# Kernel tuning notes

Measured on AMD Instinct MI355X. Metric: run time of the kernel, lower is better.

Reference implementation:

```python
import jax, jax.numpy as jnp
import numpy as np

FEAT = 32   # feature_dim
OUT = 4     # out_dim
RES = 128   # resolution per dim (D=H=W)
DO, HO, WO = 1, 2048, 1024  # query point layout


def setup_inputs() -> dict:
    key = jax.random.key(0)
    ks = jax.random.split(key, 10)
    grid = jax.random.uniform(ks[0], (1, FEAT, RES, RES, RES), dtype=jnp.float32)
    coordinate = jax.random.uniform(ks[1], (1, DO, HO, WO, 3), dtype=jnp.float32,
                                    minval=-1.0, maxval=1.0)

    def lin_w(k, fan_in, fan_out):
        # init_weights_normal: normal init scaled by 1/sqrt(fan_in)
        return jax.random.normal(k, (fan_out, fan_in), jnp.float32) * (1.0 / np.sqrt(fan_in))

    w1 = lin_w(ks[2], FEAT, FEAT); b1 = jnp.zeros((FEAT,), jnp.float32)
    w2 = lin_w(ks[3], FEAT, FEAT); b2 = jnp.zeros((FEAT,), jnp.float32)
    w3 = lin_w(ks[4], FEAT, FEAT); b3 = jnp.zeros((FEAT,), jnp.float32)
    w4 = lin_w(ks[5], FEAT, OUT);  b4 = jnp.zeros((OUT,), jnp.float32)
    return {"coordinate": coordinate, "grid": grid,
            "w1": w1, "b1": b1, "w2": w2, "b2": b2,
            "w3": w3, "b3": b3, "w4": w4, "b4": b4}


def _grid_sample3d(grid, coord):
    # grid: (1, C, D, H, W); coord: (1, Do, Ho, Wo, 3) xyz in [-1,1]
    # Matches torch F.grid_sample(mode='bilinear', padding_mode='zeros', align_corners=False)
    # Returns channels-last (1, Do, Ho, Wo, C) (== torch output permuted 0,2,3,4,1).
    _, C, D, H, W = grid.shape
    g = jnp.transpose(grid[0], (1, 2, 3, 0))  # (D, H, W, C)
    out_shape = coord.shape[:-1]
    pts = coord.reshape(-1, 3)
    x, y, z = pts[:, 0], pts[:, 1], pts[:, 2]
    # unnormalize, align_corners=False
    fx = ((x + 1.0) * W - 1.0) * 0.5
    fy = ((y + 1.0) * H - 1.0) * 0.5
    fz = ((z + 1.0) * D - 1.0) * 0.5
    x0f = jnp.floor(fx); y0f = jnp.floor(fy); z0f = jnp.floor(fz)
    tx = fx - x0f; ty = fy - y0f; tz = fz - z0f
    x0 = x0f.astype(jnp.int32); x1 = x0 + 1
    y0 = y0f.astype(jnp.int32); y1 = y0 + 1
    z0 = z0f.astype(jnp.int32); z1 = z0 + 1

    def fetch(zi, yi, xi):
        valid = ((xi >= 0) & (xi < W) & (yi >= 0) & (yi < H) & (zi >= 0) & (zi < D))
        v = g[jnp.clip(zi, 0, D - 1), jnp.clip(yi, 0, H - 1), jnp.clip(xi, 0, W - 1)]  # (N, C)
        return v * valid[:, None].astype(v.dtype)

    wx0, wx1 = (1.0 - tx)[:, None], tx[:, None]
    wy0, wy1 = (1.0 - ty)[:, None], ty[:, None]
    wz0, wz1 = (1.0 - tz)[:, None], tz[:, None]
    out = (fetch(z0, y0, x0) * (wz0 * wy0 * wx0) + fetch(z0, y0, x1) * (wz0 * wy0 * wx1)
         + fetch(z0, y1, x0) * (wz0 * wy1 * wx0) + fetch(z0, y1, x1) * (wz0 * wy1 * wx1)
         + fetch(z1, y0, x0) * (wz1 * wy0 * wx0) + fetch(z1, y0, x1) * (wz1 * wy0 * wx1)
         + fetch(z1, y1, x0) * (wz1 * wy1 * wx0) + fetch(z1, y1, x1) * (wz1 * wy1 * wx1))
    return out.reshape(*out_shape, C)


def reference(coordinate, grid, w1, b1, w2, b2, w3, b3, w4, b4):
    v = _grid_sample3d(grid, coordinate)          # (1, Do, Ho, Wo, FEAT)
    v = jax.nn.relu(v @ w1.T + b1)
    v = jax.nn.relu(v @ w2.T + b2)
    v = jax.nn.relu(v @ w3.T + b3)
    v = v @ w4.T + b4                             # (1, Do, Ho, Wo, OUT)
    return v
```

## Files before the change

kernel.cpp:

```cpp
#include <hip/hip_runtime.h>
#include <cstdint>
#include <cstddef>

#define RES   128
#define FEAT  32
#define NPTS  (2048 * 1024)
#define PLANE ((size_t)RES * RES * RES)

static __device__ __forceinline__ unsigned short f32_to_bf16_rn(float f) {
    unsigned int u = __float_as_uint(f);
    u = (u + 0x7fffu + ((u >> 16) & 1u)) >> 16;
    return (unsigned short)u;
}
static __device__ __forceinline__ float bf16_lo(unsigned int u) {
    return __uint_as_float(u << 16);
}
static __device__ __forceinline__ float bf16_hi(unsigned int u) {
    return __uint_as_float(u & 0xffff0000u);
}

__global__ __launch_bounds__(256) void transpose_grid_kernel(
    const float* __restrict__ g, unsigned short* __restrict__ out)
{
    __shared__ unsigned short lds[64][33];
    const int t  = blockIdx.x;
    const int x0 = (t & 1) * 64;
    const int y  = (t >> 1) & (RES - 1);
    const int z  = t >> 8;
    const int lane = threadIdx.x & 63;
    const int cg   = threadIdx.x >> 6;
    const size_t base = ((size_t)z * RES + y) * RES + x0;

#pragma unroll
    for (int k = 0; k < 8; ++k) {
        const int c = k * 4 + cg;
        const float v = g[(size_t)c * PLANE + base + lane];
        lds[lane][c] = f32_to_bf16_rn(v);
    }
    __syncthreads();

    const int x  = threadIdx.x >> 2;
    const int c0 = (threadIdx.x & 3) * 8;
    const unsigned short* s = &lds[x][c0];
    uint4 pk;
    pk.x = (unsigned int)s[0] | ((unsigned int)s[1] << 16);
    pk.y = (unsigned int)s[2] | ((unsigned int)s[3] << 16);
    pk.z = (unsigned int)s[4] | ((unsigned int)s[5] << 16);
    pk.w = (unsigned int)s[6] | ((unsigned int)s[7] << 16);
    uint4* outv = (uint4*)(out + base * FEAT);
    outv[threadIdx.x] = pk;
}

template <int MODE>
__global__ __launch_bounds__(256) void field_kernel(
    const float* __restrict__ coord,
    const float* __restrict__ grid,
    const unsigned short* __restrict__ tg,
    const float* __restrict__ w1, const float* __restrict__ b1,
    const float* __restrict__ w2, const float* __restrict__ b2,
    const float* __restrict__ w3, const float* __restrict__ b3,
    const float* __restrict__ w4, const float* __restrict__ b4,
    float* __restrict__ out)
{
    const int p = blockIdx.x * 256 + threadIdx.x;

    const float cx = coord[3 * p + 0];
    const float cy = coord[3 * p + 1];
    const float cz = coord[3 * p + 2];

    const float fx = ((cx + 1.0f) * (float)RES - 1.0f) * 0.5f;
    const float fy = ((cy + 1.0f) * (float)RES - 1.0f) * 0.5f;
    const float fz = ((cz + 1.0f) * (float)RES - 1.0f) * 0.5f;

    const float x0f = floorf(fx), y0f = floorf(fy), z0f = floorf(fz);
    const float tx = fx - x0f, ty = fy - y0f, tz = fz - z0f;
    const int x0 = (int)x0f, y0 = (int)y0f, z0 = (int)z0f;

    const float wxa[2] = {1.0f - tx, tx};
    const float wya[2] = {1.0f - ty, ty};
    const float wza[2] = {1.0f - tz, tz};
    const int   xia[2] = {x0, x0 + 1};
    const int   yia[2] = {y0, y0 + 1};
    const int   zia[2] = {z0, z0 + 1};

    float v[FEAT];
#pragma unroll
    for (int c = 0; c < FEAT; ++c) v[c] = 0.0f;

#pragma unroll
    for (int corner = 0; corner < 8; ++corner) {
        const int dx = corner & 1, dy = (corner >> 1) & 1, dz = corner >> 2;
        const int xi = xia[dx], yi = yia[dy], zi = zia[dz];
        const bool valid = (xi >= 0) & (xi < RES) & (yi >= 0) & (yi < RES) &
                           (zi >= 0) & (zi < RES);
        float w = wxa[dx] * wya[dy] * wza[dz];
        w = valid ? w : 0.0f;
        const int xc = min(max(xi, 0), RES - 1);
        const int yc = min(max(yi, 0), RES - 1);
        const int zc = min(max(zi, 0), RES - 1);
        const size_t vox = ((size_t)zc * RES + yc) * RES + xc;

        if (MODE == 1) {
            const uint4* cp = (const uint4*)(tg + vox * FEAT);
#pragma unroll
            for (int q = 0; q < 4; ++q) {
                const uint4 u = cp[q];
                v[q * 8 + 0] = fmaf(w, bf16_lo(u.x), v[q * 8 + 0]);
                v[q * 8 + 1] = fmaf(w, bf16_hi(u.x), v[q * 8 + 1]);
                v[q * 8 + 2] = fmaf(w, bf16_lo(u.y), v[q * 8 + 2]);
                v[q * 8 + 3] = fmaf(w, bf16_hi(u.y), v[q * 8 + 3]);
                v[q * 8 + 4] = fmaf(w, bf16_lo(u.z), v[q * 8 + 4]);
                v[q * 8 + 5] = fmaf(w, bf16_hi(u.z), v[q * 8 + 5]);
                v[q * 8 + 6] = fmaf(w, bf16_lo(u.w), v[q * 8 + 6]);
                v[q * 8 + 7] = fmaf(w, bf16_hi(u.w), v[q * 8 + 7]);
            }
        } else {
#pragma unroll
            for (int c = 0; c < FEAT; ++c)
                v[c] = fmaf(w, grid[(size_t)c * PLANE + vox], v[c]);
        }
    }

    float h[FEAT];
#pragma unroll
    for (int j = 0; j < FEAT; ++j) {
        float a = b1[j];
#pragma unroll
        for (int i = 0; i < FEAT; ++i) a = fmaf(v[i], w1[j * FEAT + i], a);
        h[j] = fmaxf(a, 0.0f);
    }
#pragma unroll
    for (int j = 0; j < FEAT; ++j) {
        float a = b2[j];
#pragma unroll
        for (int i = 0; i < FEAT; ++i) a = fmaf(h[i], w2[j * FEAT + i], a);
        v[j] = fmaxf(a, 0.0f);
    }
#pragma unroll
    for (int j = 0; j < FEAT; ++j) {
        float a = b3[j];
#pragma unroll
        for (int i = 0; i < FEAT; ++i) a = fmaf(v[i], w3[j * FEAT + i], a);
        h[j] = fmaxf(a, 0.0f);
    }
    float r[4];
#pragma unroll
    for (int o = 0; o < 4; ++o) {
        float a = b4[o];
#pragma unroll
        for (int i = 0; i < FEAT; ++i) a = fmaf(h[i], w4[o * FEAT + i], a);
        r[o] = a;
    }
    ((float4*)out)[p] = make_float4(r[0], r[1], r[2], r[3]);
}

extern "C" void kernel_launch(void* const* d_in, const int* in_sizes, int n_in,
                              void* d_out, int out_size, void* d_ws, size_t ws_size,
                              hipStream_t stream)
{
    const float* coord = (const float*)d_in[0];
    const float* grid  = (const float*)d_in[1];
    const float* w1 = (const float*)d_in[2];
    const float* b1 = (const float*)d_in[3];
    const float* w2 = (const float*)d_in[4];
    const float* b2 = (const float*)d_in[5];
    const float* w3 = (const float*)d_in[6];
    const float* b3 = (const float*)d_in[7];
    const float* w4 = (const float*)d_in[8];
    const float* b4 = (const float*)d_in[9];
    float* out = (float*)d_out;

    const size_t need = PLANE * FEAT * sizeof(unsigned short);
    if (ws_size >= need) {
        transpose_grid_kernel<<<32768, 256, 0, stream>>>(grid, (unsigned short*)d_ws);
        field_kernel<1><<<NPTS / 256, 256, 0, stream>>>(
            coord, grid, (const unsigned short*)d_ws,
            w1, b1, w2, b2, w3, b3, w4, b4, out);
    } else {
        field_kernel<0><<<NPTS / 256, 256, 0, stream>>>(
            coord, grid, (const unsigned short*)d_ws,
            w1, b1, w2, b2, w3, b3, w4, b4, out);
    }
}
```

Before: 805.9 us.

## Bin query points by spatial cell before sampling to improve gather locality

Adds a histogram, prefix scan and scatter pass that counting-sorts query points into 8^3-voxel cells, then runs the field kernel over the sorted records and writes results back to their original indices. Block indices are also swizzled across XCDs. The goal is to make the random 64-byte corner gathers from the bf16 channels-last grid hit in cache, since uniformly random points otherwise touch the whole 128 MB volume. The cost is three extra kernels, atomics, a 32 MB record buffer, scattered output stores, and a need for a larger workspace.

```diff
diff --git a/kernel.cpp b/kernel.cpp
--- a/kernel.cpp
+++ b/kernel.cpp
@@ -6,6 +6,7 @@
 #define FEAT  32
 #define NPTS  (2048 * 1024)
 #define PLANE ((size_t)RES * RES * RES)
+#define NCELL 4096
 
 static __device__ __forceinline__ unsigned short f32_to_bf16_rn(float f) {
     unsigned int u = __float_as_uint(f);
@@ -17,6 +18,21 @@
 }
 static __device__ __forceinline__ float bf16_hi(unsigned int u) {
     return __uint_as_float(u & 0xffff0000u);
+}
+static __device__ __forceinline__ void coord_to_fxyz(
+    const float* __restrict__ coord, int p, float& fx, float& fy, float& fz) {
+    const float cx = coord[3 * p + 0];
+    const float cy = coord[3 * p + 1];
+    const float cz = coord[3 * p + 2];
+    fx = ((cx + 1.0f) * (float)RES - 1.0f) * 0.5f;
+    fy = ((cy + 1.0f) * (float)RES - 1.0f) * 0.5f;
+    fz = ((cz + 1.0f) * (float)RES - 1.0f) * 0.5f;
+}
+static __device__ __forceinline__ int cell_key(float fx, float fy, float fz) {
+    const int kx = min(max((int)floorf(fx), 0), RES - 1) >> 3;
+    const int ky = min(max((int)floorf(fy), 0), RES - 1) >> 3;
+    const int kz = min(max((int)floorf(fz), 0), RES - 1) >> 3;
+    return (kz << 8) | (ky << 4) | kx;
 }
 
 __global__ __launch_bounds__(256) void transpose_grid_kernel(
@@ -34,8 +50,7 @@
 #pragma unroll
     for (int k = 0; k < 8; ++k) {
         const int c = k * 4 + cg;
-        const float v = g[(size_t)c * PLANE + base + lane];
-        lds[lane][c] = f32_to_bf16_rn(v);
+        lds[lane][c] = f32_to_bf16_rn(g[(size_t)c * PLANE + base + lane]);
     }
     __syncthreads();
 
@@ -47,8 +62,161 @@
     pk.y = (unsigned int)s[2] | ((unsigned int)s[3] << 16);
     pk.z = (unsigned int)s[4] | ((unsigned int)s[5] << 16);
     pk.w = (unsigned int)s[6] | ((unsigned int)s[7] << 16);
-    uint4* outv = (uint4*)(out + base * FEAT);
-    outv[threadIdx.x] = pk;
+    ((uint4*)(out + base * FEAT))[threadIdx.x] = pk;
+}
+
+__global__ __launch_bounds__(256) void hist_kernel(
+    const float* __restrict__ coord, unsigned* __restrict__ cnt)
+{
+    __shared__ unsigned h[NCELL];
+    for (int i = threadIdx.x; i < NCELL; i += 256) h[i] = 0;
+    __syncthreads();
+    const int stride = gridDim.x * 256;
+    for (int p = blockIdx.x * 256 + threadIdx.x; p < NPTS; p += stride) {
+        float fx, fy, fz;
+        coord_to_fxyz(coord, p, fx, fy, fz);
+        atomicAdd(&h[cell_key(fx, fy, fz)], 1u);
+    }
+    __syncthreads();
+    for (int i = threadIdx.x; i < NCELL; i += 256) {
+        const unsigned v = h[i];
+        if (v) atomicAdd(&cnt[i], v);
+    }
+}
+
+__global__ __launch_bounds__(1024) void scan_kernel(
+    const unsigned* __restrict__ cnt, unsigned* __restrict__ cursor)
+{
+    __shared__ unsigned s[1024];
+    const int t = threadIdx.x;
+    const unsigned a0 = cnt[4 * t + 0], a1 = cnt[4 * t + 1];
+    const unsigned a2 = cnt[4 * t + 2], a3 = cnt[4 * t + 3];
+    const unsigned sum = a0 + a1 + a2 + a3;
+    s[t] = sum;
+    __syncthreads();
+    for (int off = 1; off < 1024; off <<= 1) {
+        const unsigned v   = s[t];
+        const unsigned add = (t >= off) ? s[t - off] : 0u;
+        __syncthreads();
+        s[t] = v + add;
+        __syncthreads();
+    }
+    const unsigned excl = s[t] - sum;
+    cursor[4 * t + 0] = excl;
+    cursor[4 * t + 1] = excl + a0;
+    cursor[4 * t + 2] = excl + a0 + a1;
+    cursor[4 * t + 3] = excl + a0 + a1 + a2;
+}
+
+__global__ __launch_bounds__(256) void scatter_kernel(
+    const float* __restrict__ coord, unsigned* __restrict__ cursor,
+    uint4* __restrict__ rec)
+{
+    const int p = blockIdx.x * 256 + threadIdx.x;
+    float fx, fy, fz;
+    coord_to_fxyz(coord, p, fx, fy, fz);
+    const unsigned pos = atomicAdd(&cursor[cell_key(fx, fy, fz)], 1u);
+    uint4 r;
+    r.x = __float_as_uint(fx);
+    r.y = __float_as_uint(fy);
+    r.z = __float_as_uint(fz);
+    r.w = (unsigned)p;
+    rec[pos] = r;
+}
+
+__global__ __launch_bounds__(256) void field_sorted_kernel(
+    const uint4* __restrict__ rec,
+    const unsigned short* __restrict__ tg,
+    const float* __restrict__ w1, const float* __restrict__ b1,
+    const float* __restrict__ w2, const float* __restrict__ b2,
+    const float* __restrict__ w3, const float* __restrict__ b3,
+    const float* __restrict__ w4, const float* __restrict__ b4,
+    float* __restrict__ out)
+{
+    const int nblk = gridDim.x;
+    const int wg   = (blockIdx.x & 7) * (nblk >> 3) + (blockIdx.x >> 3);
+    const int p    = wg * 256 + threadIdx.x;
+
+    const uint4 r = rec[p];
+    const float fx = __uint_as_float(r.x);
+    const float fy = __uint_as_float(r.y);
+    const float fz = __uint_as_float(r.z);
+    const unsigned idx = r.w;
+
+    const float x0f = floorf(fx), y0f = floorf(fy), z0f = floorf(fz);
+    const float tx = fx - x0f, ty = fy - y0f, tz = fz - z0f;
+    const int x0 = (int)x0f, y0 = (int)y0f, z0 = (int)z0f;
+
+    const float wxa[2] = {1.0f - tx, tx};
+    const float wya[2] = {1.0f - ty, ty};
+    const float wza[2] = {1.0f - tz, tz};
+    const int   xia[2] = {x0, x0 + 1};
+    const int   yia[2] = {y0, y0 + 1};
+    const int   zia[2] = {z0, z0 + 1};
+
+    float v[FEAT];
+#pragma unroll
+    for (int c = 0; c < FEAT; ++c) v[c] = 0.0f;
+
+#pragma unroll
+    for (int corner = 0; corner < 8; ++corner) {
+        const int dx = corner & 1, dy = (corner >> 1) & 1, dz = corner >> 2;
+        const int xi = xia[dx], yi = yia[dy], zi = zia[dz];
+        const bool valid = (xi >= 0) & (xi < RES) & (yi >= 0) & (yi < RES) &
+                           (zi >= 0) & (zi < RES);
+        float w = wxa[dx] * wya[dy] * wza[dz];
+        w = valid ? w : 0.0f;
+        const int xc = min(max(xi, 0), RES - 1);
+        const int yc = min(max(yi, 0), RES - 1);
+        const int zc = min(max(zi, 0), RES - 1);
+        const size_t vox = ((size_t)zc * RES + yc) * RES + xc;
+
+        const uint4* cp = (const uint4*)(tg + vox * FEAT);
+#pragma unroll
+        for (int q = 0; q < 4; ++q) {
+            const uint4 u = cp[q];
+            v[q * 8 + 0] = fmaf(w, bf16_lo(u.x), v[q * 8 + 0]);
+            v[q * 8 + 1] = fmaf(w, bf16_hi(u.x), v[q * 8 + 1]);
+            v[q * 8 + 2] = fmaf(w, bf16_lo(u.y), v[q * 8 + 2]);
+            v[q * 8 + 3] = fmaf(w, bf16_hi(u.y), v[q * 8 + 3]);
+            v[q * 8 + 4] = fmaf(w, bf16_lo(u.z), v[q * 8 + 4]);
+            v[q * 8 + 5] = fmaf(w, bf16_hi(u.z), v[q * 8 + 5]);
+            v[q * 8 + 6] = fmaf(w, bf16_lo(u.w), v[q * 8 + 6]);
+            v[q * 8 + 7] = fmaf(w, bf16_hi(u.w), v[q * 8 + 7]);
+        }
+    }
+
+    float h[FEAT];
+#pragma unroll
+    for (int j = 0; j < FEAT; ++j) {
+        float a = b1[j];
+#pragma unroll
+        for (int i = 0; i < FEAT; ++i) a = fmaf(v[i], w1[j * FEAT + i], a);
+        h[j] = fmaxf(a, 0.0f);
+    }
+#pragma unroll
+    for (int j = 0; j < FEAT; ++j) {
+        float a = b2[j];
+#pragma unroll
+        for (int i = 0; i < FEAT; ++i) a = fmaf(h[i], w2[j * FEAT + i], a);
+        v[j] = fmaxf(a, 0.0f);
+    }
+#pragma unroll
+    for (int j = 0; j < FEAT; ++j) {
+        float a = b3[j];
+#pragma unroll
+        for (int i = 0; i < FEAT; ++i) a = fmaf(v[i], w3[j * FEAT + i], a);
+        h[j] = fmaxf(a, 0.0f);
+    }
+    float rr[4];
+#pragma unroll
+    for (int o = 0; o < 4; ++o) {
+        float a = b4[o];
+#pragma unroll
+        for (int i = 0; i < FEAT; ++i) a = fmaf(h[i], w4[o * FEAT + i], a);
+        rr[o] = a;
+    }
+    ((float4*)out)[idx] = make_float4(rr[0], rr[1], rr[2], rr[3]);
 }
 
 template <int MODE>
@@ -63,14 +231,8 @@
     float* __restrict__ out)
 {
     const int p = blockIdx.x * 256 + threadIdx.x;
-
-    const float cx = coord[3 * p + 0];
-    const float cy = coord[3 * p + 1];
-    const float cz = coord[3 * p + 2];
-
-    const float fx = ((cx + 1.0f) * (float)RES - 1.0f) * 0.5f;
-    const float fy = ((cy + 1.0f) * (float)RES - 1.0f) * 0.5f;
-    const float fz = ((cz + 1.0f) * (float)RES - 1.0f) * 0.5f;
+    float fx, fy, fz;
+    coord_to_fxyz(coord, p, fx, fy, fz);
 
     const float x0f = floorf(fx), y0f = floorf(fy), z0f = floorf(fz);
     const float tx = fx - x0f, ty = fy - y0f, tz = fz - z0f;
@@ -143,15 +305,15 @@
         for (int i = 0; i < FEAT; ++i) a = fmaf(v[i], w3[j * FEAT + i], a);
         h[j] = fmaxf(a, 0.0f);
     }
-    float r[4];
+    float rr[4];
 #pragma unroll
     for (int o = 0; o < 4; ++o) {
         float a = b4[o];
 #pragma unroll
         for (int i = 0; i < FEAT; ++i) a = fmaf(h[i], w4[o * FEAT + i], a);
-        r[o] = a;
-    }
-    ((float4*)out)[p] = make_float4(r[0], r[1], r[2], r[3]);
+        rr[o] = a;
+    }
+    ((float4*)out)[p] = make_float4(rr[0], rr[1], rr[2], rr[3]);
 }
 
 extern "C" void kernel_launch(void* const* d_in, const int* in_sizes, int n_in,
@@ -170,15 +332,34 @@
     const float* b4 = (const float*)d_in[9];
     float* out = (float*)d_out;
 
-    const size_t need = PLANE * FEAT * sizeof(unsigned short);
-    if (ws_size >= need) {
-        transpose_grid_kernel<<<32768, 256, 0, stream>>>(grid, (unsigned short*)d_ws);
+    const size_t TG_BYTES  = PLANE * FEAT * sizeof(unsigned short);
+    const size_t REC_BYTES = (size_t)NPTS * 16;
+    const size_t CNT_BYTES = NCELL * sizeof(unsigned);
+    const size_t off_rec    = TG_BYTES;
+    const size_t off_cnt    = off_rec + REC_BYTES;
+    const size_t off_cursor = off_cnt + CNT_BYTES;
+    const size_t need_sorted = off_cursor + CNT_BYTES;
+
+    unsigned short* tg = (unsigned short*)d_ws;
+
+    if (ws_size >= need_sorted) {
+        uint4*    rec    = (uint4*)((char*)d_ws + off_rec);
+        unsigned* cnt    = (unsigned*)((char*)d_ws + off_cnt);
+        unsigned* cursor = (unsigned*)((char*)d_ws + off_cursor);
+
+        transpose_grid_kernel<<<32768, 256, 0, stream>>>(grid, tg);
+        hipMemsetAsync(cnt, 0, CNT_BYTES, stream);
+        hist_kernel<<<2048, 256, 0, stream>>>(coord, cnt);
+        scan_kernel<<<1, 1024, 0, stream>>>(cnt, cursor);
+        scatter_kernel<<<NPTS / 256, 256, 0, stream>>>(coord, cursor, rec);
+        field_sorted_kernel<<<NPTS / 256, 256, 0, stream>>>(
+            rec, tg, w1, b1, w2, b2, w3, b3, w4, b4, out);
+    } else if (ws_size >= TG_BYTES) {
+        transpose_grid_kernel<<<32768, 256, 0, stream>>>(grid, tg);
         field_kernel<1><<<NPTS / 256, 256, 0, stream>>>(
-            coord, grid, (const unsigned short*)d_ws,
-            w1, b1, w2, b2, w3, b3, w4, b4, out);
+            coord, grid, tg, w1, b1, w2, b2, w3, b3, w4, b4, out);
     } else {
         field_kernel<0><<<NPTS / 256, 256, 0, stream>>>(
-            coord, grid, (const unsigned short*)d_ws,
-            w1, b1, w2, b2, w3, b3, w4, b4, out);
-    }
-}
+            coord, grid, tg, w1, b1, w2, b2, w3, b3, w4, b4, out);
+    }
+}
```

New measurement: 1.063 ms. 31.9% more time.
